# Performance work log

Measured on AMD Instinct MI355X. Metric: run time of the kernel, lower is better.

The kernel has to match this reference:

```python
import jax, jax.numpy as jnp
import numpy as np

D_MODEL = 1024
NHEAD = 16
HEAD_DIM = D_MODEL // NHEAD


def setup_inputs() -> dict:
    key = jax.random.key(0)
    k1, k2, k3 = jax.random.split(key, 3)
    x = jax.random.normal(k1, (4, 2048, D_MODEL), dtype=jnp.float32)
    # xavier_uniform init for weights, zero bias
    lim_qkv = float(np.sqrt(6.0 / (D_MODEL + 3 * D_MODEL)))
    w_qkv = jax.random.uniform(k2, (3 * D_MODEL, D_MODEL), jnp.float32, -lim_qkv, lim_qkv)
    b_qkv = jnp.zeros((3 * D_MODEL,), jnp.float32)
    lim_o = float(np.sqrt(6.0 / (D_MODEL + D_MODEL)))
    w_o = jax.random.uniform(k3, (D_MODEL, D_MODEL), jnp.float32, -lim_o, lim_o)
    b_o = jnp.zeros((D_MODEL,), jnp.float32)
    return {"x": x, "w_qkv": w_qkv, "b_qkv": b_qkv, "w_o": w_o, "b_o": b_o}


def reference(x, w_qkv, b_qkv, w_o, b_o):
    B, S, _ = x.shape
    qkv = x @ w_qkv.T + b_qkv                      # [B,S,3D]
    qkv = qkv.reshape(B, S, NHEAD, 3 * HEAD_DIM).transpose(0, 2, 1, 3)  # [B,H,S,3d]
    q, k, v = jnp.split(qkv, 3, axis=-1)           # each [B,H,S,d]
    scale = 1.0 / jnp.sqrt(jnp.asarray(HEAD_DIM, x.dtype))
    logits = jnp.einsum('bhqd,bhkd->bhqk', q, k) * scale
    attn = jax.nn.softmax(logits, axis=-1)
    vals = jnp.einsum('bhqk,bhkd->bhqd', attn, v)  # [B,H,S,d]
    vals = vals.transpose(0, 2, 1, 3).reshape(B, S, D_MODEL)
    return vals @ w_o.T + b_o
```

## Files before the change

### kernel.cpp

```cpp
#include <hip/hip_runtime.h>
#include <hip/hip_bf16.h>
#include <stdint.h>

typedef unsigned short u16;
typedef uint32_t u32;
typedef __bf16 bf16x8 __attribute__((ext_vector_type(8)));
typedef __bf16 bf16x2v __attribute__((ext_vector_type(2)));
typedef float f32x2 __attribute__((ext_vector_type(2)));
typedef float f32x4 __attribute__((ext_vector_type(4)));
typedef float f32x16 __attribute__((ext_vector_type(16)));
typedef u16 u16x4v __attribute__((ext_vector_type(4)));
typedef u32 u32x2 __attribute__((ext_vector_type(2)));

#define AS1 __attribute__((address_space(1)))
#define AS3 __attribute__((address_space(3)))

__device__ __forceinline__ void gld_lds16(const u16* g, u16* l) {
    __builtin_amdgcn_global_load_lds((const AS1 uint32_t*)g, (AS3 uint32_t*)l, 16, 0, 0);
}

__device__ __forceinline__ u16 f2bf(float f) {
    union { float f; uint32_t u; } v; v.f = f;
    uint32_t u = v.u;
    return (u16)((u + 0x7FFFu + ((u >> 16) & 1u)) >> 16);
}

__device__ __forceinline__ u32 pkbf16(float lo, float hi) {
    f32x2 e; e[0] = lo; e[1] = hi;
    union { bf16x2v b; u32 d; } u;
    u.b = __builtin_convertvector(e, bf16x2v);
    return u.d;
}

__device__ __forceinline__ u32x2 pl32swap(u32 a, u32 b) {
#if __has_builtin(__builtin_amdgcn_permlane32_swap)
    return __builtin_amdgcn_permlane32_swap(a, b, false, false);
#else
    asm volatile("v_permlane32_swap_b32 %0, %1" : "+v"(a), "+v"(b));
    u32x2 r; r[0] = a; r[1] = b; return r;
#endif
}

__device__ __forceinline__ void smpack(const f32x16& sv, f32x2& la,
                                       bf16x8& A0v, bf16x8& A1v) {
    u32 pk[8];
#pragma unroll
    for (int p = 0; p < 8; ++p) {
        const float e0 = __builtin_amdgcn_exp2f(sv[2 * p]);
        const float e1 = __builtin_amdgcn_exp2f(sv[2 * p + 1]);
        f32x2 e2; e2[0] = e0; e2[1] = e1;
        la += e2;
        pk[p] = pkbf16(e0, e1);
    }
    const u32x2 r02 = pl32swap(pk[0], pk[2]);
    const u32x2 r13 = pl32swap(pk[1], pk[3]);
    const u32x2 r46 = pl32swap(pk[4], pk[6]);
    const u32x2 r57 = pl32swap(pk[5], pk[7]);
    union { u32 d[4]; bf16x8 v; } A0, A1;
    A0.d[0] = r02[0]; A0.d[1] = r13[0]; A0.d[2] = r02[1]; A0.d[3] = r13[1];
    A1.d[0] = r46[0]; A1.d[1] = r57[0]; A1.d[2] = r46[1]; A1.d[3] = r57[1];
    A0v = A0.v; A1v = A1.v;
}

#define QSCALE 0.18033688011112042f

__global__ void cast_f32_bf16(const float* __restrict__ in, u16* __restrict__ out, int n4) {
    int i = blockIdx.x * blockDim.x + threadIdx.x;
    if (i < n4) {
        float4 f = ((const float4*)in)[i];
        u16x4v o;
        o.x = f2bf(f.x); o.y = f2bf(f.y); o.z = f2bf(f.z); o.w = f2bf(f.w);
        ((u16x4v*)out)[i] = o;
    }
}

template <int MODE>
__global__ __launch_bounds__(256, 3) void gemm_bt(
    const u16* __restrict__ A, const u16* __restrict__ B,
    const float* __restrict__ bias, float* __restrict__ Cf,
    u16* __restrict__ qb, u16* __restrict__ kb, u16* __restrict__ vT,
    int K, int ldc)
{
    __shared__ __align__(16) u16 As[128 * 64];
    __shared__ __align__(16) u16 Bs[128 * 64];
    const int tid = threadIdx.x;
    const int lane = tid & 63;
    const int w = tid >> 6;
    const int wm = (w >> 1) << 6;
    const int wn = (w & 1) << 6;
    const int r = lane & 15;
    const int q = lane >> 4;

    const int nwgx = gridDim.x;
    const int flat = blockIdx.y * nwgx + blockIdx.x;
    const int cpx = (nwgx * gridDim.y) >> 3;
    const int swz = (flat & 7) * cpx + (flat >> 3);
    const int m0 = (swz / nwgx) << 7;
    const int n0 = (swz % nwgx) << 7;

    const f32x4 zero4 = {0.f, 0.f, 0.f, 0.f};
    f32x4 acc[4][4];
#pragma unroll
    for (int i = 0; i < 4; ++i)
#pragma unroll
        for (int j = 0; j < 4; ++j) acc[i][j] = zero4;

    const int nk = K >> 6;
    for (int kt = 0; kt < nk; ++kt) {
        const int kk = kt << 6;
#pragma unroll
        for (int p = 0; p < 4; ++p) {
            const int idx = (p << 8) + tid;
            const int row = idx >> 3;
            const int cg = ((idx & 7) - row) & 7;
            gld_lds16(A + (m0 + row) * K + kk + (cg << 3), &As[idx << 3]);
            gld_lds16(B + (n0 + row) * K + kk + (cg << 3), &Bs[idx << 3]);
        }
        __syncthreads();
#pragma unroll
        for (int s = 0; s < 2; ++s) {
            bf16x8 af[4], bf[4];
#pragma unroll
            for (int i = 0; i < 4; ++i) {
                const int ra = wm + (i << 4) + r;
                af[i] = *(const bf16x8*)&As[(ra << 6) + ((((s << 2) + q + ra) & 7) << 3)];
                const int rb = wn + (i << 4) + r;
                bf[i] = *(const bf16x8*)&Bs[(rb << 6) + ((((s << 2) + q + rb) & 7) << 3)];
            }
#pragma unroll
            for (int i = 0; i < 4; ++i)
#pragma unroll
                for (int j = 0; j < 4; ++j)
                    acc[i][j] = __builtin_amdgcn_mfma_f32_16x16x32_bf16(af[i], bf[j], acc[i][j], 0, 0, 0);
        }
        __syncthreads();
    }

#pragma unroll
    for (int j = 0; j < 4; ++j) {
        const int col = n0 + wn + (j << 4) + r;
        const float bv = bias[col];
        if (MODE == 0) {
#pragma unroll
            for (int i = 0; i < 4; ++i)
#pragma unroll
                for (int ii = 0; ii < 4; ++ii) {
                    const int rowg = m0 + wm + (i << 4) + (q << 2) + ii;
                    Cf[rowg * ldc + col] = acc[i][j][ii] + bv;
                }
        } else {
            const int c0 = n0 + wn + (j << 4);
            const int h = c0 / 192;
            const int rem = c0 - h * 192;
            const int region = rem >> 6;
            const int colp = (h << 6) + (rem - (region << 6)) + r;
            if (region == 0) {
#pragma unroll
                for (int i = 0; i < 4; ++i)
#pragma unroll
                    for (int ii = 0; ii < 4; ++ii) {
                        const int rowg = m0 + wm + (i << 4) + (q << 2) + ii;
                        qb[rowg * 1024 + colp] = f2bf((acc[i][j][ii] + bv) * QSCALE);
                    }
            } else if (region == 1) {
#pragma unroll
                for (int i = 0; i < 4; ++i)
#pragma unroll
                    for (int ii = 0; ii < 4; ++ii) {
                        const int rowg = m0 + wm + (i << 4) + (q << 2) + ii;
                        kb[rowg * 1024 + colp] = f2bf(acc[i][j][ii] + bv);
                    }
            } else {
#pragma unroll
                for (int i = 0; i < 4; ++i) {
                    const int rowg0 = m0 + wm + (i << 4) + (q << 2);
                    u16x4v vv;
                    vv.x = f2bf(acc[i][j][0] + bv);
                    vv.y = f2bf(acc[i][j][1] + bv);
                    vv.z = f2bf(acc[i][j][2] + bv);
                    vv.w = f2bf(acc[i][j][3] + bv);
                    *(u16x4v*)&vT[(size_t)colp * 8192 + rowg0] = vv;
                }
            }
        }
    }
}

__global__ __launch_bounds__(256, 2) void attn(
    const u16* __restrict__ qb, const u16* __restrict__ kb,
    const u16* __restrict__ vT, u16* __restrict__ vals)
{
    __shared__ __align__(16) u16 S[16384];

    const int tid  = threadIdx.x;
    const int lane = tid & 63;
    const int w    = tid >> 6;
    const int c    = lane & 31;
    const int h2   = lane >> 5;
    const int head = blockIdx.x;
    const int q0   = blockIdx.y << 8;
    const int b    = blockIdx.z;
    const size_t rowbase = (size_t)b * 2048;

#pragma unroll
    for (int p = 0; p < 8; ++p) {
        const int idx = (p << 8) + tid;
        const int row = idx >> 3;
        const int cg  = ((idx & 7) - row) & 7;
        gld_lds16(qb + (rowbase + q0 + row) * 1024 + (head << 6) + (cg << 3), &S[idx << 3]);
    }
    __syncthreads();

    bf16x8 bq[4][2];
#pragma unroll
    for (int nt = 0; nt < 2; ++nt) {
        const int qr = (w << 6) + (nt << 5) + c;
#pragma unroll
        for (int dc = 0; dc < 4; ++dc)
            bq[dc][nt] = *(const bf16x8*)&S[(qr << 6) + ((((dc << 1) + h2 + qr) & 7) << 3)];
    }
    __syncthreads();

    const int srow8 = tid >> 3;
    const int scg   = ((tid & 7) - srow8) & 7;
    const u16* gK = kb + (rowbase + srow8) * 1024 + (head << 6) + (scg << 3);
    const u16* gV = vT + (size_t)((head << 6) + srow8) * 8192 + rowbase + (scg << 3);

    {
        u16* buf = S + 8192;
        gld_lds16(gK,             &buf[tid << 3]);
        gld_lds16(gK + 32 * 1024, &buf[2048 + (tid << 3)]);
        gld_lds16(gV,             &buf[4096 + (tid << 3)]);
        gld_lds16(gV + 32 * 8192, &buf[6144 + (tid << 3)]);
    }
    __syncthreads();

    int aF[4];
#pragma unroll
    for (int i = 0; i < 4; ++i)
        aF[i] = (c << 6) + ((((i << 1) + h2 + c) & 7) << 3);

    f32x16 oacc[2][2];
    f32x2 la2[2];
    f32x16 zero16;
#pragma unroll
    for (int i = 0; i < 16; ++i) {
        zero16[i] = 0.f;
        oacc[0][0][i] = 0.f; oacc[0][1][i] = 0.f;
        oacc[1][0][i] = 0.f; oacc[1][1][i] = 0.f;
    }
    la2[0][0] = 0.f; la2[0][1] = 0.f;
    la2[1][0] = 0.f; la2[1][1] = 0.f;

    const u16* gKr = gK + 65536;
    const u16* gVr = gV + 64;

    for (int kt = 0; kt < 32; ++kt) {
        const int cur = kt & 1;
        if (kt > 0) __syncthreads();
        u16* bufP = (cur == 0) ? (S + 0) : (S + 8192);
        const u16* bufC = (cur == 0) ? (S + 8192) : (S + 0);
        if (kt < 31) {
            gld_lds16(gKr,             &bufP[tid << 3]);
            gld_lds16(gKr + 32 * 1024, &bufP[2048 + (tid << 3)]);
            gld_lds16(gVr,             &bufP[4096 + (tid << 3)]);
            gld_lds16(gVr + 32 * 8192, &bufP[6144 + (tid << 3)]);
            gKr += 65536;
            gVr += 64;
        }
        const u16* Ks  = bufC;
        const u16* VTs = bufC + 4096;

#pragma unroll
        for (int mt = 0; mt < 2; ++mt) {
            __builtin_amdgcn_s_setprio(1);
            const bf16x8 ak0 = *(const bf16x8*)&Ks[aF[0] + (mt << 11)];
            f32x16 s0 = __builtin_amdgcn_mfma_f32_32x32x16_bf16(ak0, bq[0][0], zero16, 0, 0, 0);
            f32x16 s1 = __builtin_amdgcn_mfma_f32_32x32x16_bf16(ak0, bq[0][1], zero16, 0, 0, 0);
#pragma unroll
            for (int dc = 1; dc < 4; ++dc) {
                const bf16x8 ak = *(const bf16x8*)&Ks[aF[dc] + (mt << 11)];
                s0 = __builtin_amdgcn_mfma_f32_32x32x16_bf16(ak, bq[dc][0], s0, 0, 0, 0);
                s1 = __builtin_amdgcn_mfma_f32_32x32x16_bf16(ak, bq[dc][1], s1, 0, 0, 0);
            }
            __builtin_amdgcn_s_setprio(0);

            bf16x8 av[4];
#pragma unroll
            for (int ht = 0; ht < 2; ++ht)
#pragma unroll
                for (int c16 = 0; c16 < 2; ++c16)
                    av[(ht << 1) | c16] =
                        *(const bf16x8*)&VTs[aF[(mt << 1) | c16] + (ht << 11)];

#pragma unroll
            for (int nt = 0; nt < 2; ++nt) {
                const f32x16& sv = (nt == 0) ? s0 : s1;
                bf16x8 A0v, A1v;
                smpack(sv, la2[nt], A0v, A1v);

                __builtin_amdgcn_s_setprio(1);
#pragma unroll
                for (int ht = 0; ht < 2; ++ht) {
                    oacc[ht][nt] = __builtin_amdgcn_mfma_f32_32x32x16_bf16(av[(ht << 1) | 0], A0v, oacc[ht][nt], 0, 0, 0);
                    oacc[ht][nt] = __builtin_amdgcn_mfma_f32_32x32x16_bf16(av[(ht << 1) | 1], A1v, oacc[ht][nt], 0, 0, 0);
                }
                __builtin_amdgcn_s_setprio(0);
            }
        }
    }

#pragma unroll
    for (int nt = 0; nt < 2; ++nt) {
        float myl = la2[nt][0] + la2[nt][1];
        myl += __shfl_xor(myl, 32, 64);
        const float inv = 1.f / myl;
        const size_t orow = rowbase + q0 + (w << 6) + (nt << 5) + c;
#pragma unroll
        for (int ht = 0; ht < 2; ++ht)
#pragma unroll
            for (int r4 = 0; r4 < 4; ++r4) {
                u16x4v vv;
                vv.x = f2bf(oacc[ht][nt][4 * r4 + 0] * inv);
                vv.y = f2bf(oacc[ht][nt][4 * r4 + 1] * inv);
                vv.z = f2bf(oacc[ht][nt][4 * r4 + 2] * inv);
                vv.w = f2bf(oacc[ht][nt][4 * r4 + 3] * inv);
                const int hd0 = (ht << 5) + (r4 << 3) + (h2 << 2);
                *(u16x4v*)&vals[orow * 1024 + (head << 6) + hd0] = vv;
            }
    }
}

extern "C" void kernel_launch(void* const* d_in, const int* in_sizes, int n_in,
                              void* d_out, int out_size, void* d_ws, size_t ws_size,
                              hipStream_t stream) {
    (void)in_sizes; (void)n_in; (void)out_size; (void)ws_size;
    const float* x     = (const float*)d_in[0];
    const float* w_qkv = (const float*)d_in[1];
    const float* b_qkv = (const float*)d_in[2];
    const float* w_o   = (const float*)d_in[3];
    const float* b_o   = (const float*)d_in[4];
    float* out = (float*)d_out;

    char* ws = (char*)d_ws;
    u16* xb    = (u16*)(ws);
    u16* wqkvb = (u16*)(ws + (size_t)(16 << 20));
    u16* wob   = (u16*)(ws + (size_t)(22 << 20));
    u16* qb    = (u16*)(ws + (size_t)(24 << 20));
    u16* kb    = (u16*)(ws + (size_t)(40 << 20));
    u16* vTb   = (u16*)(ws + (size_t)(56 << 20));
    u16* valsb = (u16*)(ws + (size_t)(72 << 20));

    cast_f32_bf16<<<8192, 256, 0, stream>>>(x, xb, 2097152);
    cast_f32_bf16<<<3072, 256, 0, stream>>>(w_qkv, wqkvb, 786432);
    cast_f32_bf16<<<1024, 256, 0, stream>>>(w_o, wob, 262144);

    gemm_bt<1><<<dim3(24, 64), 256, 0, stream>>>(xb, wqkvb, b_qkv, nullptr,
                                                 qb, kb, vTb, 1024, 3072);

    attn<<<dim3(16, 8, 4), 256, 0, stream>>>(qb, kb, vTb, valsb);

    gemm_bt<0><<<dim3(8, 64), 256, 0, stream>>>(valsb, wob, b_o, out,
                                                nullptr, nullptr, nullptr, 1024, 1024);
}
```

Before: 262.9 us.

## Load K and V fragments directly from global memory instead of via LDS

Removes the double-buffered LDS staging of K and V^T tiles and their per-iteration barriers. Each wave now reads its MFMA operand fragments straight from global memory using per-lane pointers. This drops the __syncthreads and LDS traffic, but every wave re-fetches the same K/V data redundantly through the cache, and the global load latency is now exposed inside the compute loop with no prefetch.

```diff
diff --git a/kernel.cpp b/kernel.cpp
--- a/kernel.cpp
+++ b/kernel.cpp
@@ -219,26 +219,9 @@
         for (int dc = 0; dc < 4; ++dc)
             bq[dc][nt] = *(const bf16x8*)&S[(qr << 6) + ((((dc << 1) + h2 + qr) & 7) << 3)];
     }
-    __syncthreads();
-
-    const int srow8 = tid >> 3;
-    const int scg   = ((tid & 7) - srow8) & 7;
-    const u16* gK = kb + (rowbase + srow8) * 1024 + (head << 6) + (scg << 3);
-    const u16* gV = vT + (size_t)((head << 6) + srow8) * 8192 + rowbase + (scg << 3);
-
-    {
-        u16* buf = S + 8192;
-        gld_lds16(gK,             &buf[tid << 3]);
-        gld_lds16(gK + 32 * 1024, &buf[2048 + (tid << 3)]);
-        gld_lds16(gV,             &buf[4096 + (tid << 3)]);
-        gld_lds16(gV + 32 * 8192, &buf[6144 + (tid << 3)]);
-    }
-    __syncthreads();
-
-    int aF[4];
-#pragma unroll
-    for (int i = 0; i < 4; ++i)
-        aF[i] = (c << 6) + ((((i << 1) + h2 + c) & 7) << 3);
+
+    const u16* kp = kb + (rowbase + c) * 1024 + (head << 6) + (h2 << 3);
+    const u16* vp = vT + (size_t)((head << 6) + c) * 8192 + rowbase + (h2 << 3);
 
     f32x16 oacc[2][2];
     f32x2 la2[2];
@@ -252,36 +235,22 @@
     la2[0][0] = 0.f; la2[0][1] = 0.f;
     la2[1][0] = 0.f; la2[1][1] = 0.f;
 
-    const u16* gKr = gK + 65536;
-    const u16* gVr = gV + 64;
-
     for (int kt = 0; kt < 32; ++kt) {
-        const int cur = kt & 1;
-        if (kt > 0) __syncthreads();
-        u16* bufP = (cur == 0) ? (S + 0) : (S + 8192);
-        const u16* bufC = (cur == 0) ? (S + 8192) : (S + 0);
-        if (kt < 31) {
-            gld_lds16(gKr,             &bufP[tid << 3]);
-            gld_lds16(gKr + 32 * 1024, &bufP[2048 + (tid << 3)]);
-            gld_lds16(gVr,             &bufP[4096 + (tid << 3)]);
-            gld_lds16(gVr + 32 * 8192, &bufP[6144 + (tid << 3)]);
-            gKr += 65536;
-            gVr += 64;
-        }
-        const u16* Ks  = bufC;
-        const u16* VTs = bufC + 4096;
-
 #pragma unroll
         for (int mt = 0; mt < 2; ++mt) {
+            const u16* kpm = kp + (mt << 15);
+            bf16x8 ak[4];
+#pragma unroll
+            for (int dc = 0; dc < 4; ++dc)
+                ak[dc] = *(const bf16x8*)&kpm[dc << 4];
+
             __builtin_amdgcn_s_setprio(1);
-            const bf16x8 ak0 = *(const bf16x8*)&Ks[aF[0] + (mt << 11)];
-            f32x16 s0 = __builtin_amdgcn_mfma_f32_32x32x16_bf16(ak0, bq[0][0], zero16, 0, 0, 0);
-            f32x16 s1 = __builtin_amdgcn_mfma_f32_32x32x16_bf16(ak0, bq[0][1], zero16, 0, 0, 0);
+            f32x16 s0 = __builtin_amdgcn_mfma_f32_32x32x16_bf16(ak[0], bq[0][0], zero16, 0, 0, 0);
+            f32x16 s1 = __builtin_amdgcn_mfma_f32_32x32x16_bf16(ak[0], bq[0][1], zero16, 0, 0, 0);
 #pragma unroll
             for (int dc = 1; dc < 4; ++dc) {
-                const bf16x8 ak = *(const bf16x8*)&Ks[aF[dc] + (mt << 11)];
-                s0 = __builtin_amdgcn_mfma_f32_32x32x16_bf16(ak, bq[dc][0], s0, 0, 0, 0);
-                s1 = __builtin_amdgcn_mfma_f32_32x32x16_bf16(ak, bq[dc][1], s1, 0, 0, 0);
+                s0 = __builtin_amdgcn_mfma_f32_32x32x16_bf16(ak[dc], bq[dc][0], s0, 0, 0, 0);
+                s1 = __builtin_amdgcn_mfma_f32_32x32x16_bf16(ak[dc], bq[dc][1], s1, 0, 0, 0);
             }
             __builtin_amdgcn_s_setprio(0);
 
@@ -291,7 +260,7 @@
 #pragma unroll
                 for (int c16 = 0; c16 < 2; ++c16)
                     av[(ht << 1) | c16] =
-                        *(const bf16x8*)&VTs[aF[(mt << 1) | c16] + (ht << 11)];
+                        *(const bf16x8*)&vp[((size_t)ht << 18) + (mt << 5) + (c16 << 4)];
 
 #pragma unroll
             for (int nt = 0; nt < 2; ++nt) {
@@ -308,6 +277,8 @@
                 __builtin_amdgcn_s_setprio(0);
             }
         }
+        kp += 65536;
+        vp += 64;
     }
 
 #pragma unroll
```

Result: slower. 313.2 us (+19.1%).
